# Performance work log

Hardware: AMD Instinct MI355X
Metric: run time of the kernel (lower is better)

## Reference

```python
import jax, jax.numpy as jnp
import numpy as np

B, N = 16, 512


def _line_coords(n):
    # Discrete Fourier slice coordinates for all mValues (center=False, ridgelet=False).
    mu = n + n // 2 if n % 2 == 0 else n + 1
    p = 2 if n % 2 == 0 else n
    m = jnp.arange(mu)           # [mu]
    k = jnp.arange(n)            # [N]
    lt = (m < n)[:, None]        # m < N branch mask, [mu, 1]
    # m < N:  row = k,                 col = (k*m) % N
    # m >= N: row = (k*p*(m-N)) % N,   col = k
    row = jnp.where(lt, k[None, :], (k[None, :] * p * (m[:, None] - n)) % n)
    col = jnp.where(lt, (k[None, :] * m[:, None]) % n, k[None, :])
    return row, col  # each [mu, N] int32


def setup_inputs() -> dict:
    key = jax.random.key(0)
    return {"image": jax.random.normal(key, (B, N, N), dtype=jnp.float32)}


def reference(image):
    b, n, _ = image.shape
    row, col = _line_coords(n)                                   # [mu, N]
    dft = jnp.fft.fft2(image.astype(jnp.complex64), norm="ortho")  # [B, N, N] c64
    slices = dft[:, row, col]                                    # gather -> [B, mu, N]
    sino = jnp.fft.ifft(slices, norm="ortho")                    # [B, mu, N] c64
    # complex sinogram returned as stacked (real, imag) float channels
    return jnp.stack([sino.real, sino.imag], axis=-1)            # [B, mu, N, 2]
```

## Files before the change

kernel.cpp:

```cpp
#include <hip/hip_runtime.h>


#define NN 512
#define MU 768
#define MASK 511
#define SCALE 0.04419417382415922f

__global__ __launch_bounds__(512) void k_init(const float* __restrict__ img,
                                              float* __restrict__ A0) {
  __shared__ float T[3][64][65];
  const int bx = blockIdx.x, b = blockIdx.y;
  const int xp = bx >> 2, wt = bx & 3;
  const int x0 = xp * 64, x1 = x0 + 256, w0 = wt * 64;
  const float* src = img + (size_t)b * NN * NN;
  float* dst = A0 + (size_t)b * (512 * NN);

  auto load_tile = [&](int tile, int xb, int wb, int idx) {
    const int r = (idx >> 4) & 63, c4 = (idx & 15) << 2;
    const float4 v = *(const float4*)&src[(size_t)(xb + r) * NN + wb + c4];
    T[tile][r][c4]     = v.x;
    T[tile][r][c4 + 1] = v.y;
    T[tile][r][c4 + 2] = v.z;
    T[tile][r][c4 + 3] = v.w;
  };
  auto store2 = [&](const float (*Ta)[65], const float (*Tb)[65], int rbase,
                    int cbase) {
    for (int idx = threadIdx.x; idx < 1024; idx += 512) {
      const int wl = idx >> 4, x4 = (idx & 15) << 2;
      float4 a;
      a.x = Ta[x4][wl]     + Tb[x4][wl];
      a.y = Ta[x4 + 1][wl] + Tb[x4 + 1][wl];
      a.z = Ta[x4 + 2][wl] + Tb[x4 + 2][wl];
      a.w = Ta[x4 + 3][wl] + Tb[x4 + 3][wl];
      *(float4*)&dst[(size_t)(rbase + wl) * NN + cbase + x4] = a;
    }
  };

  for (int idx = threadIdx.x; idx < 3072; idx += 512) {
    const int tile = idx >> 10;
    load_tile(tile, (tile == 2) ? x1 : x0, (tile == 0) ? w0 : w0 + 256, idx);
  }
  __syncthreads();
  store2(T[0], T[1], w0, x0);
  store2(T[0], T[2], 256 + w0, x0);
  __syncthreads();
  for (int idx = threadIdx.x; idx < 1024; idx += 512) load_tile(0, x1, w0, idx);
  __syncthreads();
  store2(T[0], T[2], w0, x1);
  store2(T[0], T[1], 256 + w0, x1);
}

__global__ __launch_bounds__(512) void k_pass1(const float* __restrict__ A0,
                                               const float* __restrict__ img,
                                               float* __restrict__ A1,
                                               float* __restrict__ B1) {
  __shared__ float L[16 * 512];
  const int bx = blockIdx.x, b = blockIdx.y;
  const int t = threadIdx.x;
  const bool isB = bx >= 32;
  const int c = isB ? 0 : (bx >> 4);
  const int w = isB ? (bx - 32) : (bx & 15);
  if (isB) {
    const float4* s4 = (const float4*)(img + (size_t)b * NN * NN);
    float4* l4 = (float4*)L;
    for (int it = 0; it < 4; ++it) {
      int flat = it * 512 + t;
      int lrow = flat >> 7, col = flat & 127;
      float4 u = s4[(w + 16 * lrow) * 128 + col];
      float4 v = s4[(w + 16 * lrow + 256) * 128 + col];
      u.x += v.x; u.y += v.y; u.z += v.z; u.w += v.w;
      l4[lrow * 128 + col] = u;
    }
  } else {
    const float4* s4 = (const float4*)(A0 + (size_t)b * 512 * NN);
    float4* l4 = (float4*)L;
    const int pbase = c * 256 + w;
    for (int it = 0; it < 4; ++it) {
      int flat = it * 512 + t;
      int lrow = flat >> 7, col = flat & 127;
      l4[lrow * 128 + col] = s4[(pbase + 16 * lrow) * 128 + col];
    }
  }
  __syncthreads();
  const int g = t >> 7;
  const int x4 = (t & 127) * 4;
  float* outA = A1 + (size_t)b * 512 * NN;
  float* outB = B1 + (size_t)b * 256 * NN;
  for (int jj = 0; jj < 4; ++jj) {
    const int j = jj * 4 + g;
    const int C = isB ? (2 * j) : (c + 2 * j);
    float4 acc = {0.f, 0.f, 0.f, 0.f};
#pragma unroll
    for (int bb = 0; bb < 16; ++bb) {
      int base = (x4 - C * bb * 16) & MASK;
      float4 v = *(const float4*)&L[bb * 512 + base];
      acc.x += v.x; acc.y += v.y; acc.z += v.z; acc.w += v.w;
    }
    const int orow = isB ? (j * 16 + w) : (C * 16 + w);
    float* op = isB ? outB : outA;
    *(float4*)&op[(size_t)orow * NN + x4] = acc;
  }
}

__global__ __launch_bounds__(512) void k_pass2(const float* __restrict__ A1,
                                               const float* __restrict__ B1,
                                               float2* __restrict__ out) {
  __shared__ float L[16 * 512];
  const int bx = blockIdx.x, b = blockIdx.y;
  const int t = threadIdx.x;
  const bool isB = bx >= 32;
  const int c = isB ? 2 * (bx - 32) : bx;
  const float* in = isB ? (B1 + (size_t)b * 256 * NN + (size_t)(c >> 1) * 16 * NN)
                        : (A1 + (size_t)b * 512 * NN + (size_t)c * 16 * NN);
  {
    const float4* s4 = (const float4*)in;
    float4* l4 = (float4*)L;
    for (int it = 0; it < 4; ++it) l4[it * 512 + t] = s4[it * 512 + t];
  }
  __syncthreads();
  float acc[16];
#pragma unroll
  for (int j = 0; j < 16; ++j) acc[j] = 0.f;
#pragma unroll
  for (int bb = 0; bb < 16; ++bb) {
    int base = (t - c * bb) & MASK;
    const int step = (32 * bb) & MASK;
    const float* row = L + bb * 512;
#pragma unroll
    for (int j = 0; j < 16; ++j) {
      acc[j] += row[base];
      base = (base - step) & MASK;
    }
  }
#pragma unroll
  for (int j = 0; j < 16; ++j) {
    int m = isB ? (512 + (c >> 1) + 16 * j) : (c + 32 * j);
    float2 o; o.x = acc[j] * SCALE; o.y = 0.f;
    out[((size_t)b * MU + m) * NN + t] = o;
  }
}

#define TM 16
#define YT 16
#define LDS_STRIDE 516
__global__ __launch_bounds__(512) void drt_main(const float* __restrict__ img,
                                                float* __restrict__ out) {
  __shared__ float rows[YT * LDS_STRIDE];
  const int b = blockIdx.y;
  const int tile = blockIdx.x;
  const int t = threadIdx.x;
  const bool caseB = (tile >= 32);
  const int a0 = caseB ? (tile - 32) * TM : tile * TM;
  const float* __restrict__ src = img + (size_t)b * (NN * NN);
  const int slope0 = caseB ? (2 * a0) : a0;
  const int dslope = caseB ? 2 : 1;
  float acc[TM];
#pragma unroll
  for (int i = 0; i < TM; ++i) acc[i] = 0.0f;
  for (int y0 = 0; y0 < NN; y0 += YT) {
    __syncthreads();
    if (caseB) {
#pragma unroll
      for (int r = 0; r < YT; ++r) rows[r * LDS_STRIDE + t] = src[(y0 + r) * NN + t];
    } else {
#pragma unroll
      for (int rep = 0; rep < YT; ++rep) {
        int idx = rep * NN + t;
        int xx = idx >> 4, cc = idx & 15;
        rows[cc * LDS_STRIDE + xx] = src[xx * NN + y0 + cc];
      }
    }
    __syncthreads();
#pragma unroll 4
    for (int r = 0; r < YT; ++r) {
      const int v = y0 + r;
      int base = t - slope0 * v;
      const int step = dslope * v;
      const float* __restrict__ rowp = rows + r * LDS_STRIDE;
#pragma unroll
      for (int i = 0; i < TM; ++i) { acc[i] += rowp[base & MASK]; base -= step; }
    }
  }
  const int m = caseB ? (NN + a0) : a0;
  float2* outp = (float2*)out;
#pragma unroll
  for (int i = 0; i < TM; ++i) {
    float2 vv; vv.x = acc[i] * SCALE; vv.y = 0.0f;
    outp[((size_t)b * MU + (m + i)) * NN + t] = vv;
  }
}

extern "C" void kernel_launch(void* const* d_in, const int* in_sizes, int n_in,
                              void* d_out, int out_size, void* d_ws, size_t ws_size,
                              hipStream_t stream) {
  const float* img = (const float*)d_in[0];
  if (ws_size < (size_t)42 * 1024 * 1024) {
    drt_main<<<dim3(48, 16), dim3(512), 0, stream>>>(img, (float*)d_out);
    return;
  }
  float* W  = (float*)d_ws;
  float* A0 = W;
  float* A1 = W + 4194304;
  float* B1 = W + 8388608;

  k_init <<<dim3(16, 16), dim3(512), 0, stream>>>(img, A0);
  k_pass1<<<dim3(48, 16), dim3(512), 0, stream>>>(A0, img, A1, B1);
  k_pass2<<<dim3(48, 16), dim3(512), 0, stream>>>(A1, B1, (float2*)d_out);
}
```

Measured before the change: 99.03 us.

## Fuse three passes into one cooperative kernel with grid-wide syncs

Merges the init, pass1 and pass2 kernels into a single cooperative launch of 768 blocks, using grid.sync between the stages, with one shared buffer reused by all three. The goal is to remove two kernel launch boundaries and their drain and ramp-up gaps. It checks occupancy once and falls back to the three separate launches if a cooperative launch is not possible. Grid syncs carry their own cost, and the launch bounds may limit registers.

```diff
diff --git a/kernel.cpp b/kernel.cpp
--- a/kernel.cpp
+++ b/kernel.cpp
@@ -1,4 +1,7 @@
 #include <hip/hip_runtime.h>
+#include <hip/hip_cooperative_groups.h>
+
+namespace cg = cooperative_groups;
 
 
 #define NN 512
@@ -6,10 +9,10 @@
 #define MASK 511
 #define SCALE 0.04419417382415922f
 
-__global__ __launch_bounds__(512) void k_init(const float* __restrict__ img,
-                                              float* __restrict__ A0) {
-  __shared__ float T[3][64][65];
-  const int bx = blockIdx.x, b = blockIdx.y;
+__device__ __forceinline__ void init_body(int b, int bx, int t, float* S,
+                                          const float* __restrict__ img,
+                                          float* __restrict__ A0) {
+  float (*T)[64][65] = (float (*)[64][65])S;
   const int xp = bx >> 2, wt = bx & 3;
   const int x0 = xp * 64, x1 = x0 + 256, w0 = wt * 64;
   const float* src = img + (size_t)b * NN * NN;
@@ -25,7 +28,7 @@
   };
   auto store2 = [&](const float (*Ta)[65], const float (*Tb)[65], int rbase,
                     int cbase) {
-    for (int idx = threadIdx.x; idx < 1024; idx += 512) {
+    for (int idx = t; idx < 1024; idx += 512) {
       const int wl = idx >> 4, x4 = (idx & 15) << 2;
       float4 a;
       a.x = Ta[x4][wl]     + Tb[x4][wl];
@@ -36,7 +39,7 @@
     }
   };
 
-  for (int idx = threadIdx.x; idx < 3072; idx += 512) {
+  for (int idx = t; idx < 3072; idx += 512) {
     const int tile = idx >> 10;
     load_tile(tile, (tile == 2) ? x1 : x0, (tile == 0) ? w0 : w0 + 256, idx);
   }
@@ -44,19 +47,17 @@
   store2(T[0], T[1], w0, x0);
   store2(T[0], T[2], 256 + w0, x0);
   __syncthreads();
-  for (int idx = threadIdx.x; idx < 1024; idx += 512) load_tile(0, x1, w0, idx);
+  for (int idx = t; idx < 1024; idx += 512) load_tile(0, x1, w0, idx);
   __syncthreads();
   store2(T[0], T[2], w0, x1);
   store2(T[0], T[1], 256 + w0, x1);
 }
 
-__global__ __launch_bounds__(512) void k_pass1(const float* __restrict__ A0,
-                                               const float* __restrict__ img,
-                                               float* __restrict__ A1,
-                                               float* __restrict__ B1) {
-  __shared__ float L[16 * 512];
-  const int bx = blockIdx.x, b = blockIdx.y;
-  const int t = threadIdx.x;
+__device__ __forceinline__ void pass1_body(int b, int bx, int t, float* L,
+                                           const float* __restrict__ A0,
+                                           const float* __restrict__ img,
+                                           float* __restrict__ A1,
+                                           float* __restrict__ B1) {
   const bool isB = bx >= 32;
   const int c = isB ? 0 : (bx >> 4);
   const int w = isB ? (bx - 32) : (bx & 15);
@@ -102,12 +103,10 @@
   }
 }
 
-__global__ __launch_bounds__(512) void k_pass2(const float* __restrict__ A1,
-                                               const float* __restrict__ B1,
-                                               float2* __restrict__ out) {
-  __shared__ float L[16 * 512];
-  const int bx = blockIdx.x, b = blockIdx.y;
-  const int t = threadIdx.x;
+__device__ __forceinline__ void pass2_body(int b, int bx, int t, float* L,
+                                           const float* __restrict__ A1,
+                                           const float* __restrict__ B1,
+                                           float2* __restrict__ out) {
   const bool isB = bx >= 32;
   const int c = isB ? 2 * (bx - 32) : bx;
   const float* in = isB ? (B1 + (size_t)b * 256 * NN + (size_t)(c >> 1) * 16 * NN)
@@ -138,6 +137,40 @@
     float2 o; o.x = acc[j] * SCALE; o.y = 0.f;
     out[((size_t)b * MU + m) * NN + t] = o;
   }
+}
+
+__global__ __launch_bounds__(512, 6) void drt_fused(const float* __restrict__ img,
+                                                    float* __restrict__ A0,
+                                                    float* __restrict__ A1,
+                                                    float* __restrict__ B1,
+                                                    float2* __restrict__ out) {
+  __shared__ float S[3 * 64 * 65];
+  cg::grid_group grid = cg::this_grid();
+  const int gb = blockIdx.x, t = threadIdx.x;
+  if (gb < 256) init_body(gb >> 4, gb & 15, t, S, img, A0);
+  grid.sync();
+  pass1_body(gb / 48, gb % 48, t, S, A0, img, A1, B1);
+  grid.sync();
+  pass2_body(gb / 48, gb % 48, t, S, A1, B1, out);
+}
+
+__global__ __launch_bounds__(512) void k_init(const float* __restrict__ img,
+                                              float* __restrict__ A0) {
+  __shared__ float S[3 * 64 * 65];
+  init_body(blockIdx.y, blockIdx.x, threadIdx.x, S, img, A0);
+}
+__global__ __launch_bounds__(512) void k_pass1(const float* __restrict__ A0,
+                                               const float* __restrict__ img,
+                                               float* __restrict__ A1,
+                                               float* __restrict__ B1) {
+  __shared__ float L[16 * 512];
+  pass1_body(blockIdx.y, blockIdx.x, threadIdx.x, L, A0, img, A1, B1);
+}
+__global__ __launch_bounds__(512) void k_pass2(const float* __restrict__ A1,
+                                               const float* __restrict__ B1,
+                                               float2* __restrict__ out) {
+  __shared__ float L[16 * 512];
+  pass2_body(blockIdx.y, blockIdx.x, threadIdx.x, L, A1, B1, out);
 }
 
 #define TM 16
@@ -202,8 +235,25 @@
   float* A0 = W;
   float* A1 = W + 4194304;
   float* B1 = W + 8388608;
-
+  float2* outp = (float2*)d_out;
+
+  static int coopOk = -1;
+  if (coopOk < 0) {
+    int nb = 0;
+    hipError_t qe = hipOccupancyMaxActiveBlocksPerMultiprocessor(
+        &nb, (const void*)drt_fused, 512, 0);
+    coopOk = (qe == hipSuccess && nb >= 3) ? 1 : 0;
+  }
+  if (coopOk == 1) {
+    void* args[] = {(void*)&img, (void*)&A0, (void*)&A1, (void*)&B1,
+                    (void*)&outp};
+    hipError_t e = hipLaunchCooperativeKernel((const void*)drt_fused,
+                                              dim3(768), dim3(512), args, 0,
+                                              stream);
+    if (e == hipSuccess) return;
+    coopOk = 0;
+  }
   k_init <<<dim3(16, 16), dim3(512), 0, stream>>>(img, A0);
   k_pass1<<<dim3(48, 16), dim3(512), 0, stream>>>(A0, img, A1, B1);
-  k_pass2<<<dim3(48, 16), dim3(512), 0, stream>>>(A1, B1, (float2*)d_out);
-}
+  k_pass2<<<dim3(48, 16), dim3(512), 0, stream>>>(A1, B1, outp);
+}
```

New measurement: 102.5 us. 1.04x slower.
